# Optimization experiments

Hardware: AMD Instinct MI355X
Metric: run time of the kernel (lower is better)

The kernel has to match this reference:

```python
import jax, jax.numpy as jnp
import numpy as np

D, H, HKV, DH, F, E = 2048, 16, 4, 128, 2048, 8
EPS, THETA = 1e-5, 500000.0
B, S = 1, 512


def _rms(x, w):
    return x * jax.lax.rsqrt(jnp.mean(x * x, -1, keepdims=True) + EPS) * w


def _rope(q, k, pos):
    inv = 1.0 / (THETA ** (jnp.arange(0, DH, 2, dtype=jnp.float32) / DH))
    f = pos.astype(jnp.float32)[..., None] * inv            # (B,S,DH/2)
    cos = jnp.concatenate([jnp.cos(f)] * 2, -1)[:, None]    # (B,1,S,DH)
    sin = jnp.concatenate([jnp.sin(f)] * 2, -1)[:, None]
    def rot(x):
        x1, x2 = jnp.split(x, 2, -1)
        return jnp.concatenate([-x2, x1], -1)
    return q * cos + rot(q) * sin, k * cos + rot(k) * sin


def _forward(hidden_states, attention_mask, position_ids, attn_norm_w, wq, wk, wv, wo,
             ffn_norm_w, router_w, w_gate, w_up, w_down, ws_gate, ws_up, ws_down):
    b, s, _ = hidden_states.shape
    # --- attention block ---
    x = _rms(hidden_states, attn_norm_w)
    q = (x @ wq).reshape(b, s, H, DH).transpose(0, 2, 1, 3)     # (B,H,S,DH)
    k = (x @ wk).reshape(b, s, HKV, DH).transpose(0, 2, 1, 3)   # (B,HKV,S,DH)
    v = (x @ wv).reshape(b, s, HKV, DH).transpose(0, 2, 1, 3)
    q, k = _rope(q, k, position_ids)
    k = jnp.repeat(k, H // HKV, axis=1)
    v = jnp.repeat(v, H // HKV, axis=1)
    scores = jnp.einsum('bhqd,bhkd->bhqk', q, k) / np.float32(np.sqrt(DH))
    causal = jnp.tril(jnp.ones((s, s), bool))
    mask = causal[None, None] & (attention_mask[:, None, None, :] > 0)
    scores = jnp.where(mask, scores, jnp.float32(-1e9))
    p = jax.nn.softmax(scores, axis=-1)
    attn = jnp.einsum('bhqk,bhkd->bhqd', p, v).transpose(0, 2, 1, 3).reshape(b, s, H * DH) @ wo
    h = hidden_states + attn
    # --- MoE block (layer_id even): top-1 sigmoid routing, score scales expert input; shared expert always on ---
    x2 = _rms(h, ffn_norm_w)
    logits = x2 @ router_w                                      # (B,S,E)
    top_idx = jnp.argmax(logits, -1)
    top_score = jax.nn.sigmoid(jnp.max(logits, -1))
    gates = jax.nn.one_hot(top_idx, E, dtype=x2.dtype) * top_score[..., None]  # (B,S,E)
    xin = jnp.einsum('bse,bsd->ebsd', gates, x2)                # scaled dispatch
    g = jax.nn.silu(jnp.einsum('ebsd,edf->ebsf', xin, w_gate))
    u = jnp.einsum('ebsd,edf->ebsf', xin, w_up)
    routed = jnp.einsum('ebsf,efd->bsd', g * u, w_down)
    shared = (jax.nn.silu(x2 @ ws_gate) * (x2 @ ws_up)) @ ws_down
    return h + routed + shared


def setup_inputs() -> dict:
    key = jax.random.key(0)
    ks = jax.random.split(key, 14)
    s = 0.02
    return {
        'hidden_states': jax.random.normal(ks[0], (B, S, D), jnp.float32),
        'attention_mask': jnp.ones((B, S), jnp.int32),
        'position_ids': jnp.broadcast_to(jnp.arange(S, dtype=jnp.int32)[None], (B, S)),
        'attn_norm_w': jnp.ones((D,), jnp.float32),
        'wq': jax.random.normal(ks[1], (D, H * DH), jnp.float32) * s,
        'wk': jax.random.normal(ks[2], (D, HKV * DH), jnp.float32) * s,
        'wv': jax.random.normal(ks[3], (D, HKV * DH), jnp.float32) * s,
        'wo': jax.random.normal(ks[4], (H * DH, D), jnp.float32) * s,
        'ffn_norm_w': jnp.ones((D,), jnp.float32),
        'router_w': jax.random.normal(ks[5], (D, E), jnp.float32) * s,
        'w_gate': jax.random.normal(ks[6], (E, D, F), jnp.float32) * s,
        'w_up': jax.random.normal(ks[7], (E, D, F), jnp.float32) * s,
        'w_down': jax.random.normal(ks[8], (E, F, D), jnp.float32) * s,
        'ws_gate': jax.random.normal(ks[9], (D, F), jnp.float32) * s,
        'ws_up': jax.random.normal(ks[10], (D, F), jnp.float32) * s,
        'ws_down': jax.random.normal(ks[11], (F, D), jnp.float32) * s,
    }


def reference(hidden_states, attention_mask, position_ids, attn_norm_w, wq, wk, wv, wo,
              ffn_norm_w, router_w, w_gate, w_up, w_down, ws_gate, ws_up, ws_down):
    return _forward(hidden_states, attention_mask, position_ids, attn_norm_w, wq, wk, wv, wo,
                    ffn_norm_w, router_w, w_gate, w_up, w_down, ws_gate, ws_up, ws_down)
```

## Files before the change

kernel.cpp:

```cpp
#include <hip/hip_runtime.h>
#include <cstdint>
#include <cstddef>

#define S_LEN 512
#define DMODEL 2048
#define NH 16
#define NKVH 4
#define DHEAD 128
#define FFD 2048
#define NEXP 8

typedef __attribute__((ext_vector_type(8))) short s8v;
typedef __attribute__((ext_vector_type(4))) float f4v;

__device__ __forceinline__ unsigned short f2bf(float f) {
    unsigned int u = __float_as_uint(f);
    unsigned int r = u + 0x7fffu + ((u >> 16) & 1u);
    return (unsigned short)(r >> 16);
}
__device__ __forceinline__ float bf2f(unsigned short h) {
    return __uint_as_float(((unsigned int)h) << 16);
}

__device__ __forceinline__ f4v mfma_bf16(s8v a, s8v b, f4v c) {
    return __builtin_amdgcn_mfma_f32_16x16x32_bf16(a, b, c, 0, 0, 0);
}

__global__ __launch_bounds__(256) void rms_pair_k(const float* __restrict__ x,
                                                  const float* __restrict__ w,
                                                  unsigned short* __restrict__ hi,
                                                  unsigned short* __restrict__ lo) {
    int row = blockIdx.x;
    const float* xr = x + (size_t)row * DMODEL;
    float ss = 0.f;
    for (int i = threadIdx.x; i < DMODEL; i += 256) { float v = xr[i]; ss = fmaf(v, v, ss); }
    for (int off = 32; off > 0; off >>= 1) ss += __shfl_xor(ss, off);
    __shared__ float red[4];
    if ((threadIdx.x & 63) == 0) red[threadIdx.x >> 6] = ss;
    __syncthreads();
    float tot = (red[0] + red[1]) + (red[2] + red[3]);
    float scale = 1.0f / sqrtf(tot * (1.0f / DMODEL) + 1e-5f);
    for (int i = threadIdx.x; i < DMODEL; i += 256) {
        float v = xr[i] * scale * w[i];
        unsigned short hb = f2bf(v);
        hi[(size_t)row * DMODEL + i] = hb;
        lo[(size_t)row * DMODEL + i] = f2bf(v - bf2f(hb));
    }
}

__global__ __launch_bounds__(256) void rms_dual_k(const float* __restrict__ x,
                                                  const float* __restrict__ w,
                                                  float* __restrict__ xf,
                                                  unsigned short* __restrict__ xb) {
    int row = blockIdx.x;
    const float* xr = x + (size_t)row * DMODEL;
    float ss = 0.f;
    for (int i = threadIdx.x; i < DMODEL; i += 256) { float v = xr[i]; ss = fmaf(v, v, ss); }
    for (int off = 32; off > 0; off >>= 1) ss += __shfl_xor(ss, off);
    __shared__ float red[4];
    if ((threadIdx.x & 63) == 0) red[threadIdx.x >> 6] = ss;
    __syncthreads();
    float tot = (red[0] + red[1]) + (red[2] + red[3]);
    float scale = 1.0f / sqrtf(tot * (1.0f / DMODEL) + 1e-5f);
    for (int i = threadIdx.x; i < DMODEL; i += 256) {
        float v = xr[i] * scale * w[i];
        xf[(size_t)row * DMODEL + i] = v;
        xb[(size_t)row * DMODEL + i] = f2bf(v);
    }
}

template <bool SPLIT>
__global__ __launch_bounds__(256) void gemm2_k(const unsigned short* __restrict__ Ahi,
                                               const unsigned short* __restrict__ Alo,
                                               const float* __restrict__ B0,
                                               const float* __restrict__ B1,
                                               float* __restrict__ C0,
                                               float* __restrict__ C1,
                                               int M, int N, int nE, int KS,
                                               const int* __restrict__ lists,
                                               const int* __restrict__ counts,
                                               long long bstride) {
    __shared__ unsigned short Ah[64][40];
    __shared__ unsigned short Al[SPLIT ? 64 : 1][40];
    __shared__ unsigned short Bt[64][40];
    __shared__ unsigned short Bl[SPLIT ? 64 : 1][40];

    int z = blockIdx.z;
    int e = 0;
    if (nE > 1) { e = z % nE; z /= nE; }
    int which = 0;
    if (B1 != nullptr) { which = z & 1; z >>= 1; }
    const int ks = z;

    int myM = M;
    const int* rl = nullptr;
    if (lists) { rl = lists + e * S_LEN; myM = counts[e]; }
    const int m0 = blockIdx.y * 64;
    if (m0 >= myM) return;

    const float* Bp = (which ? B1 : B0) + (long long)e * bstride;
    float* Cp = which ? C1 : C0;
    const int n0 = blockIdx.x * 64;

    const int tid = threadIdx.x;
    const int ar = tid >> 2;
    const int ak = (tid & 3) << 3;
    const int bn = tid & 63;
    const int bk8 = (tid >> 6) << 3;
    const int bc = ((bk8 >> 3) ^ (bn >> 3)) & 3;

    const int arow = m0 + ar;
    const bool avalid = arow < myM;
    const int arow_g = avalid ? (rl ? rl[arow] : arow) : 0;

    const unsigned short* Ahp = Ahi + (size_t)arow_g * DMODEL + ak;
    const unsigned short* Alp = SPLIT ? (Alo + (size_t)arow_g * DMODEL + ak) : nullptr;

    const int lane = tid & 63;
    const int wv = tid >> 6;
    const int wm = wv >> 1;
    const int wn = wv & 1;
    const int lr = lane & 15;
    const int quad = lane >> 4;

    f4v zero = {0.f, 0.f, 0.f, 0.f};
    f4v acc[2][2];
    acc[0][0] = zero; acc[0][1] = zero; acc[1][0] = zero; acc[1][1] = zero;

    const int kslice = DMODEL / KS;
    const int kbeg = ks * kslice;
    const int niter = kslice >> 5;

    for (int it = 0; it < niter; ++it) {
        const int k0 = kbeg + (it << 5);
        uint4 hv = {0, 0, 0, 0};
        uint4 lv = {0, 0, 0, 0};
        if (avalid) {
            hv = *(const uint4*)(Ahp + k0);
            if constexpr (SPLIT) lv = *(const uint4*)(Alp + k0);
        }
        const float* bp = Bp + (size_t)(k0 + bk8) * N + n0 + bn;
        float f[8];
#pragma unroll
        for (int j = 0; j < 8; j++) f[j] = bp[(size_t)j * N];
        unsigned int ph[4], pl[4];
#pragma unroll
        for (int j = 0; j < 4; j++) {
            unsigned short h0 = f2bf(f[2 * j]), h1 = f2bf(f[2 * j + 1]);
            ph[j] = (unsigned int)h0 | ((unsigned int)h1 << 16);
            if constexpr (SPLIT) {
                unsigned short l0 = f2bf(f[2 * j] - bf2f(h0));
                unsigned short l1 = f2bf(f[2 * j + 1] - bf2f(h1));
                pl[j] = (unsigned int)l0 | ((unsigned int)l1 << 16);
            }
        }
        __syncthreads();
        *(uint4*)&Ah[ar][ak] = hv;
        if constexpr (SPLIT) *(uint4*)&Al[ar][ak] = lv;
        *(uint4*)&Bt[bn][bc << 3] = *(uint4*)ph;
        if constexpr (SPLIT) *(uint4*)&Bl[bn][bc << 3] = *(uint4*)pl;
        __syncthreads();
        const int br0 = wn * 32 + lr, br1 = wn * 32 + 16 + lr;
        const int c0 = ((quad ^ (br0 >> 3)) & 3) << 3;
        const int c1 = ((quad ^ (br1 >> 3)) & 3) << 3;
        s8v ah0 = *(const s8v*)&Ah[wm * 32 + lr][quad * 8];
        s8v ah1 = *(const s8v*)&Ah[wm * 32 + 16 + lr][quad * 8];
        s8v bh0 = *(const s8v*)&Bt[br0][c0];
        s8v bh1 = *(const s8v*)&Bt[br1][c1];
        acc[0][0] = mfma_bf16(ah0, bh0, acc[0][0]);
        acc[0][1] = mfma_bf16(ah0, bh1, acc[0][1]);
        acc[1][0] = mfma_bf16(ah1, bh0, acc[1][0]);
        acc[1][1] = mfma_bf16(ah1, bh1, acc[1][1]);
        if constexpr (SPLIT) {
            s8v al0 = *(const s8v*)&Al[wm * 32 + lr][quad * 8];
            s8v al1 = *(const s8v*)&Al[wm * 32 + 16 + lr][quad * 8];
            s8v bl0 = *(const s8v*)&Bl[br0][c0];
            s8v bl1 = *(const s8v*)&Bl[br1][c1];
            acc[0][0] = mfma_bf16(ah0, bl0, acc[0][0]);
            acc[0][0] = mfma_bf16(al0, bh0, acc[0][0]);
            acc[0][1] = mfma_bf16(ah0, bl1, acc[0][1]);
            acc[0][1] = mfma_bf16(al0, bh1, acc[0][1]);
            acc[1][0] = mfma_bf16(ah1, bl0, acc[1][0]);
            acc[1][0] = mfma_bf16(al1, bh0, acc[1][0]);
            acc[1][1] = mfma_bf16(ah1, bl1, acc[1][1]);
            acc[1][1] = mfma_bf16(al1, bh1, acc[1][1]);
        }
    }
#pragma unroll
    for (int t = 0; t < 2; t++) {
#pragma unroll
        for (int u = 0; u < 2; u++) {
#pragma unroll
            for (int r2 = 0; r2 < 4; r2++) {
                int rml = m0 + wm * 32 + t * 16 + quad * 4 + r2;
                if (rml >= myM) continue;
                int rg = rl ? rl[rml] : rml;
                int col = n0 + wn * 32 + u * 16 + lr;
                atomicAdd(&Cp[(size_t)rg * N + col], acc[t][u][r2]);
            }
        }
    }
}

__global__ __launch_bounds__(256) void rope_k(float* __restrict__ qb, float* __restrict__ kb,
                                              const int* __restrict__ pos_ids) {
    int idx = blockIdx.x * 256 + threadIdx.x;
    int i = idx & 63;
    int rest = idx >> 6;
    int head = rest % (NH + NKVH);
    int s = rest / (NH + NKVH);
    if (s >= S_LEN) return;
    float pos = (float)pos_ids[s];
    float inv = (float)exp(-(double)i * (log(500000.0) / 64.0));
    float f = pos * inv;
    float c = cosf(f), sn = sinf(f);
    float* p;
    if (head < NH) p = qb + (size_t)s * (NH * DHEAD) + head * DHEAD;
    else p = kb + (size_t)s * (NKVH * DHEAD) + (head - NH) * DHEAD;
    float x1 = p[i], x2 = p[i + 64];
    p[i] = x1 * c - x2 * sn;
    p[i + 64] = x2 * c + x1 * sn;
}

__global__ __launch_bounds__(256) void attn_k(const float* __restrict__ qb,
                                              const float* __restrict__ kb,
                                              const float* __restrict__ vb,
                                              const int* __restrict__ amask,
                                              unsigned short* __restrict__ ohi,
                                              unsigned short* __restrict__ olo) {
    __shared__ float KV[64][133];
    __shared__ float Qs[16][133];
    __shared__ float Ps[4][4][64];
    const int qt = blockIdx.x;
    const int h = blockIdx.y;
    const int kvh = h >> 2;
    const int tid = threadIdx.x;
    const int w = tid >> 6;
    const int lane = tid & 63;
    const float qsc = 0.08838834764831845f;

    for (int i = tid; i < 16 * 128; i += 256) {
        int r = i >> 7, d = i & 127;
        Qs[r][d] = qb[(size_t)(qt * 16 + r) * (NH * DHEAD) + h * DHEAD + d] * qsc;
    }
    float m_i[4], l_i[4], o0[4], o1[4];
#pragma unroll
    for (int r = 0; r < 4; r++) { m_i[r] = -3.0e38f; l_i[r] = 0.f; o0[r] = 0.f; o1[r] = 0.f; }
    const int ntiles = ((qt * 16 + 15) >> 6) + 1;
    __syncthreads();
    for (int kt = 0; kt < ntiles; kt++) {
        for (int i = tid; i < 64 * 128; i += 256) {
            int r = i >> 7, d = i & 127;
            KV[r][d] = kb[(size_t)(kt * 64 + r) * (NKVH * DHEAD) + kvh * DHEAD + d];
        }
        __syncthreads();
        const int kg = kt * 64 + lane;
        const bool kvalid = (amask[kg] > 0);
        float sc[4] = {0.f, 0.f, 0.f, 0.f};
        for (int d = 0; d < 128; d++) {
            float kval = KV[lane][d];
#pragma unroll
            for (int r = 0; r < 4; r++) sc[r] = fmaf(Qs[w * 4 + r][d], kval, sc[r]);
        }
#pragma unroll
        for (int r = 0; r < 4; r++) {
            const int qg = qt * 16 + w * 4 + r;
            float sr = (kvalid && kg <= qg) ? sc[r] : -1.0e30f;
            float mt = sr;
            for (int off = 32; off > 0; off >>= 1) mt = fmaxf(mt, __shfl_xor(mt, off));
            float mn = fmaxf(m_i[r], mt);
            float p = expf(sr - mn);
            float alpha = expf(m_i[r] - mn);
            float psum = p;
            for (int off = 32; off > 0; off >>= 1) psum += __shfl_xor(psum, off);
            l_i[r] = l_i[r] * alpha + psum;
            m_i[r] = mn;
            o0[r] *= alpha; o1[r] *= alpha;
            Ps[w][r][lane] = p;
        }
        __syncthreads();
        for (int i = tid; i < 64 * 128; i += 256) {
            int r = i >> 7, d = i & 127;
            KV[r][d] = vb[(size_t)(kt * 64 + r) * (NKVH * DHEAD) + kvh * DHEAD + d];
        }
        __syncthreads();
#pragma unroll 4
        for (int j = 0; j < 64; j++) {
            float v0 = KV[j][lane];
            float v1 = KV[j][lane + 64];
#pragma unroll
            for (int r = 0; r < 4; r++) {
                float p = Ps[w][r][j];
                o0[r] = fmaf(p, v0, o0[r]);
                o1[r] = fmaf(p, v1, o1[r]);
            }
        }
        __syncthreads();
    }
#pragma unroll
    for (int r = 0; r < 4; r++) {
        const int qg = qt * 16 + w * 4 + r;
        float linv = 1.0f / l_i[r];
        float a0 = o0[r] * linv, a1 = o1[r] * linv;
        size_t base = (size_t)qg * (NH * DHEAD) + h * DHEAD;
        unsigned short h0 = f2bf(a0), h1 = f2bf(a1);
        ohi[base + lane] = h0;
        ohi[base + lane + 64] = h1;
        olo[base + lane] = f2bf(a0 - bf2f(h0));
        olo[base + lane + 64] = f2bf(a1 - bf2f(h1));
    }
}

__global__ __launch_bounds__(256) void router_k(const float* __restrict__ x2f,
                                                const float* __restrict__ rw,
                                                float* __restrict__ logits) {
    int t = blockIdx.x;
    int e = threadIdx.x >> 5;
    int j = threadIdx.x & 31;
    const float* xr = x2f + (size_t)t * DMODEL;
    float p = 0.f;
    for (int k = j; k < DMODEL; k += 32) p = fmaf(xr[k], rw[(size_t)k * NEXP + e], p);
    for (int off = 16; off > 0; off >>= 1) p += __shfl_xor(p, off);
    if (j == 0) logits[t * NEXP + e] = p;
}

__global__ __launch_bounds__(512) void route_build_k(const float* __restrict__ logits,
                                                     float* __restrict__ tscore,
                                                     int* __restrict__ counts,
                                                     int* __restrict__ lists) {
    int t = threadIdx.x;
    const float* lg = logits + t * NEXP;
    int best = 0;
    float bv = lg[0];
#pragma unroll
    for (int e = 1; e < NEXP; e++) { float v = lg[e]; if (v > bv) { bv = v; best = e; } }
    tscore[t] = 1.0f / (1.0f + expf(-bv));
    int pos = atomicAdd(&counts[best], 1);
    lists[best * S_LEN + pos] = t;
}

__global__ __launch_bounds__(256) void silu_shared_k(const float* __restrict__ G,
                                                     const float* __restrict__ U,
                                                     unsigned short* __restrict__ o) {
    int i = blockIdx.x * 256 + threadIdx.x;
    float g = G[i], u = U[i];
    o[i] = f2bf(g / (1.0f + expf(-g)) * u);
}

__global__ __launch_bounds__(256) void silu_routed_k(const float* __restrict__ G,
                                                     const float* __restrict__ U,
                                                     const float* __restrict__ tscore,
                                                     unsigned short* __restrict__ o) {
    int i = blockIdx.x * 256 + threadIdx.x;
    int t = i >> 11;
    float s = tscore[t];
    float g = s * G[i], u = s * U[i];
    o[i] = f2bf(g / (1.0f + expf(-g)) * u);
}

extern "C" void kernel_launch(void* const* d_in, const int* in_sizes, int n_in,
                              void* d_out, int out_size, void* d_ws, size_t ws_size,
                              hipStream_t stream) {
    const float* hidden = (const float*)d_in[0];
    const int* amask = (const int*)d_in[1];
    const int* posid = (const int*)d_in[2];
    const float* anw = (const float*)d_in[3];
    const float* wq = (const float*)d_in[4];
    const float* wk = (const float*)d_in[5];
    const float* wvv = (const float*)d_in[6];
    const float* wo = (const float*)d_in[7];
    const float* fnw = (const float*)d_in[8];
    const float* rw = (const float*)d_in[9];
    const float* wg = (const float*)d_in[10];
    const float* wu = (const float*)d_in[11];
    const float* wd = (const float*)d_in[12];
    const float* wsg = (const float*)d_in[13];
    const float* wsu = (const float*)d_in[14];
    const float* wsd = (const float*)d_in[15];
    float* out = (float*)d_out;

    char* ws = (char*)d_ws;
    size_t off = 0;
    auto alloc = [&](size_t bytes) -> void* {
        void* p = ws + off;
        off += (bytes + 255) & ~(size_t)255;
        return p;
    };
    unsigned short* x1h = (unsigned short*)alloc((size_t)S_LEN * DMODEL * 2);
    unsigned short* x1l = (unsigned short*)alloc((size_t)S_LEN * DMODEL * 2);
    float* qb = (float*)alloc((size_t)S_LEN * NH * DHEAD * 4);
    float* kb = (float*)alloc((size_t)S_LEN * NKVH * DHEAD * 4);
    float* vb = (float*)alloc((size_t)S_LEN * NKVH * DHEAD * 4);
    unsigned short* ath = (unsigned short*)alloc((size_t)S_LEN * DMODEL * 2);
    unsigned short* atl = (unsigned short*)alloc((size_t)S_LEN * DMODEL * 2);
    float* hbuf = (float*)alloc((size_t)S_LEN * DMODEL * 4);
    float* x2f = (float*)alloc((size_t)S_LEN * DMODEL * 4);
    unsigned short* x2b = (unsigned short*)alloc((size_t)S_LEN * DMODEL * 2);
    float* Gb = (float*)alloc((size_t)S_LEN * FFD * 4);
    float* Ub = (float*)alloc((size_t)S_LEN * FFD * 4);
    float* G2 = (float*)alloc((size_t)S_LEN * FFD * 4);
    float* U2 = (float*)alloc((size_t)S_LEN * FFD * 4);
    unsigned short* smid = (unsigned short*)alloc((size_t)S_LEN * FFD * 2);
    unsigned short* hmid = (unsigned short*)alloc((size_t)S_LEN * FFD * 2);
    float* logits = (float*)alloc((size_t)S_LEN * NEXP * 4);
    float* tscore = (float*)alloc((size_t)S_LEN * 4);
    int* counts = (int*)alloc(NEXP * 4);
    int* lists = (int*)alloc((size_t)NEXP * S_LEN * 4);

    const long long EXP_STRIDE = (long long)DMODEL * FFD;

    hipMemsetAsync(counts, 0, NEXP * 4, stream);
    hipMemsetAsync(qb, 0, (size_t)S_LEN * NH * DHEAD * 4, stream);
    hipMemsetAsync(kb, 0, (size_t)S_LEN * NKVH * DHEAD * 4, stream);
    hipMemsetAsync(vb, 0, (size_t)S_LEN * NKVH * DHEAD * 4, stream);
    hipMemsetAsync(Gb, 0, (size_t)S_LEN * FFD * 4, stream);
    hipMemsetAsync(Ub, 0, (size_t)S_LEN * FFD * 4, stream);
    hipMemsetAsync(G2, 0, (size_t)S_LEN * FFD * 4, stream);
    hipMemsetAsync(U2, 0, (size_t)S_LEN * FFD * 4, stream);
    hipMemcpyAsync(hbuf, hidden, (size_t)S_LEN * DMODEL * 4, hipMemcpyDeviceToDevice, stream);

    rms_pair_k<<<S_LEN, 256, 0, stream>>>(hidden, anw, x1h, x1l);
    gemm2_k<true><<<dim3(32, 8, 4), 256, 0, stream>>>(x1h, x1l, wq, nullptr, qb, nullptr,
                                                      S_LEN, 2048, 1, 4, nullptr, nullptr, 0);
    gemm2_k<true><<<dim3(8, 8, 8), 256, 0, stream>>>(x1h, x1l, wk, wvv, kb, vb,
                                                     S_LEN, 512, 1, 4, nullptr, nullptr, 0);
    rope_k<<<2560, 256, 0, stream>>>(qb, kb, posid);
    attn_k<<<dim3(32, NH), 256, 0, stream>>>(qb, kb, vb, amask, ath, atl);
    gemm2_k<true><<<dim3(32, 8, 4), 256, 0, stream>>>(ath, atl, wo, nullptr, hbuf, nullptr,
                                                      S_LEN, 2048, 1, 4, nullptr, nullptr, 0);

    rms_dual_k<<<S_LEN, 256, 0, stream>>>(hbuf, fnw, x2f, x2b);
    router_k<<<S_LEN, 256, 0, stream>>>(x2f, rw, logits);
    route_build_k<<<1, 512, 0, stream>>>(logits, tscore, counts, lists);

    hipMemcpyAsync(out, hbuf, (size_t)S_LEN * DMODEL * 4, hipMemcpyDeviceToDevice, stream);

    gemm2_k<false><<<dim3(32, 8, 8), 256, 0, stream>>>(x2b, nullptr, wsg, wsu, Gb, Ub,
                                                       S_LEN, FFD, 1, 4, nullptr, nullptr, 0);
    silu_shared_k<<<(S_LEN * FFD) / 256, 256, 0, stream>>>(Gb, Ub, smid);
    gemm2_k<false><<<dim3(32, 8, 4), 256, 0, stream>>>(smid, nullptr, wsd, nullptr, out, nullptr,
                                                       S_LEN, DMODEL, 1, 4, nullptr, nullptr, 0);

    gemm2_k<false><<<dim3(32, 8, 64), 256, 0, stream>>>(x2b, nullptr, wg, wu, G2, U2,
                                                        S_LEN, FFD, NEXP, 4, lists, counts, EXP_STRIDE);
    silu_routed_k<<<(S_LEN * FFD) / 256, 256, 0, stream>>>(G2, U2, tscore, hmid);
    gemm2_k<false><<<dim3(32, 8, 32), 256, 0, stream>>>(hmid, nullptr, wd, nullptr, out, nullptr,
                                                        S_LEN, DMODEL, NEXP, 4, lists, counts, EXP_STRIDE);
}
```

Measured before the change: 819.4 us.

## Replace atomic split-K GEMMs with partial buffers and fuse SwiGLU into gate/up GEMM

The generic split-K GEMM, which accumulated into zeroed buffers, is replaced by specialised kernels. The QKV projection runs as one launch with a 2-way K split into separate partial buffers, which are summed in rope and a v-add kernel. The routed and shared gate/up GEMMs run in a single launch with SiLU and score scaling in the epilogue, which removes the large fp32 G/U intermediates and the separate silu kernels. The down projection writes two partial buffers per path, and a final kernel sums them with the residual. This drops the memsets and memcpys and cuts global traffic, but the gate/up GEMM now loops over the full K with fewer blocks and has more live accumulators.

```diff
diff --git a/kernel.cpp b/kernel.cpp
--- a/kernel.cpp
+++ b/kernel.cpp
@@ -21,7 +21,6 @@
 __device__ __forceinline__ float bf2f(unsigned short h) {
     return __uint_as_float(((unsigned int)h) << 16);
 }
-
 __device__ __forceinline__ f4v mfma_bf16(s8v a, s8v b, f4v c) {
     return __builtin_amdgcn_mfma_f32_16x16x32_bf16(a, b, c, 0, 0, 0);
 }
@@ -48,14 +47,23 @@
     }
 }
 
-__global__ __launch_bounds__(256) void rms_dual_k(const float* __restrict__ x,
-                                                  const float* __restrict__ w,
-                                                  float* __restrict__ xf,
-                                                  unsigned short* __restrict__ xb) {
+__global__ __launch_bounds__(256) void rms_dual2_k(const float* __restrict__ hidden,
+                                                   const float* __restrict__ hs0,
+                                                   const float* __restrict__ hs1,
+                                                   const float* __restrict__ w,
+                                                   float* __restrict__ hbuf,
+                                                   float* __restrict__ xf,
+                                                   unsigned short* __restrict__ xb) {
+    __shared__ float vrow[DMODEL];
     int row = blockIdx.x;
-    const float* xr = x + (size_t)row * DMODEL;
+    size_t base = (size_t)row * DMODEL;
     float ss = 0.f;
-    for (int i = threadIdx.x; i < DMODEL; i += 256) { float v = xr[i]; ss = fmaf(v, v, ss); }
+    for (int i = threadIdx.x; i < DMODEL; i += 256) {
+        float v = hidden[base + i] + hs0[base + i] + hs1[base + i];
+        vrow[i] = v;
+        hbuf[base + i] = v;
+        ss = fmaf(v, v, ss);
+    }
     for (int off = 32; off > 0; off >>= 1) ss += __shfl_xor(ss, off);
     __shared__ float red[4];
     if ((threadIdx.x & 63) == 0) red[threadIdx.x >> 6] = ss;
@@ -63,82 +71,57 @@
     float tot = (red[0] + red[1]) + (red[2] + red[3]);
     float scale = 1.0f / sqrtf(tot * (1.0f / DMODEL) + 1e-5f);
     for (int i = threadIdx.x; i < DMODEL; i += 256) {
-        float v = xr[i] * scale * w[i];
-        xf[(size_t)row * DMODEL + i] = v;
-        xb[(size_t)row * DMODEL + i] = f2bf(v);
-    }
-}
-
-template <bool SPLIT>
-__global__ __launch_bounds__(256) void gemm2_k(const unsigned short* __restrict__ Ahi,
-                                               const unsigned short* __restrict__ Alo,
-                                               const float* __restrict__ B0,
-                                               const float* __restrict__ B1,
-                                               float* __restrict__ C0,
-                                               float* __restrict__ C1,
-                                               int M, int N, int nE, int KS,
-                                               const int* __restrict__ lists,
-                                               const int* __restrict__ counts,
-                                               long long bstride) {
+        float v = vrow[i] * scale * w[i];
+        xf[base + i] = v;
+        xb[base + i] = f2bf(v);
+    }
+}
+
+struct S3Args {
+    const unsigned short* Ahi; const unsigned short* Alo;
+    const float* B0; const float* B1; const float* B2;
+    float* C00; float* C01; float* C10; float* C11; float* C20; float* C21;
+    int N0, N1, N2;
+    int x1, x2;
+};
+
+__global__ __launch_bounds__(256) void gemm_split3_k(S3Args a) {
     __shared__ unsigned short Ah[64][40];
-    __shared__ unsigned short Al[SPLIT ? 64 : 1][40];
+    __shared__ unsigned short Al[64][40];
     __shared__ unsigned short Bt[64][40];
-    __shared__ unsigned short Bl[SPLIT ? 64 : 1][40];
-
-    int z = blockIdx.z;
-    int e = 0;
-    if (nE > 1) { e = z % nE; z /= nE; }
-    int which = 0;
-    if (B1 != nullptr) { which = z & 1; z >>= 1; }
-    const int ks = z;
-
-    int myM = M;
-    const int* rl = nullptr;
-    if (lists) { rl = lists + e * S_LEN; myM = counts[e]; }
+    __shared__ unsigned short Bl[64][40];
+
+    const int x = blockIdx.x;
+    const float* Bp; float* Cp; int N; int n0;
+    if (x < a.x1)      { Bp = a.B0; N = a.N0; n0 = x * 64;
+                         Cp = blockIdx.z ? a.C01 : a.C00; }
+    else if (x < a.x2) { Bp = a.B1; N = a.N1; n0 = (x - a.x1) * 64;
+                         Cp = blockIdx.z ? a.C11 : a.C10; }
+    else               { Bp = a.B2; N = a.N2; n0 = (x - a.x2) * 64;
+                         Cp = blockIdx.z ? a.C21 : a.C20; }
     const int m0 = blockIdx.y * 64;
-    if (m0 >= myM) return;
-
-    const float* Bp = (which ? B1 : B0) + (long long)e * bstride;
-    float* Cp = which ? C1 : C0;
-    const int n0 = blockIdx.x * 64;
+    const int kbeg = blockIdx.z * (DMODEL / 2);
 
     const int tid = threadIdx.x;
-    const int ar = tid >> 2;
-    const int ak = (tid & 3) << 3;
-    const int bn = tid & 63;
-    const int bk8 = (tid >> 6) << 3;
+    const int ar = tid >> 2, ak = (tid & 3) << 3;
+    const int bn = tid & 63, bk8 = (tid >> 6) << 3;
     const int bc = ((bk8 >> 3) ^ (bn >> 3)) & 3;
 
-    const int arow = m0 + ar;
-    const bool avalid = arow < myM;
-    const int arow_g = avalid ? (rl ? rl[arow] : arow) : 0;
-
-    const unsigned short* Ahp = Ahi + (size_t)arow_g * DMODEL + ak;
-    const unsigned short* Alp = SPLIT ? (Alo + (size_t)arow_g * DMODEL + ak) : nullptr;
-
-    const int lane = tid & 63;
-    const int wv = tid >> 6;
-    const int wm = wv >> 1;
-    const int wn = wv & 1;
-    const int lr = lane & 15;
-    const int quad = lane >> 4;
+    const unsigned short* Ahp = a.Ahi + (size_t)(m0 + ar) * DMODEL + ak;
+    const unsigned short* Alp = a.Alo + (size_t)(m0 + ar) * DMODEL + ak;
+
+    const int lane = tid & 63, wv = tid >> 6;
+    const int wm = wv >> 1, wn = wv & 1;
+    const int lr = lane & 15, quad = lane >> 4;
 
     f4v zero = {0.f, 0.f, 0.f, 0.f};
     f4v acc[2][2];
     acc[0][0] = zero; acc[0][1] = zero; acc[1][0] = zero; acc[1][1] = zero;
 
-    const int kslice = DMODEL / KS;
-    const int kbeg = ks * kslice;
-    const int niter = kslice >> 5;
-
-    for (int it = 0; it < niter; ++it) {
+    for (int it = 0; it < 32; ++it) {
         const int k0 = kbeg + (it << 5);
-        uint4 hv = {0, 0, 0, 0};
-        uint4 lv = {0, 0, 0, 0};
-        if (avalid) {
-            hv = *(const uint4*)(Ahp + k0);
-            if constexpr (SPLIT) lv = *(const uint4*)(Alp + k0);
-        }
+        uint4 hv = *(const uint4*)(Ahp + k0);
+        uint4 lv = *(const uint4*)(Alp + k0);
         const float* bp = Bp + (size_t)(k0 + bk8) * N + n0 + bn;
         float f[8];
 #pragma unroll
@@ -148,17 +131,15 @@
         for (int j = 0; j < 4; j++) {
             unsigned short h0 = f2bf(f[2 * j]), h1 = f2bf(f[2 * j + 1]);
             ph[j] = (unsigned int)h0 | ((unsigned int)h1 << 16);
-            if constexpr (SPLIT) {
-                unsigned short l0 = f2bf(f[2 * j] - bf2f(h0));
-                unsigned short l1 = f2bf(f[2 * j + 1] - bf2f(h1));
-                pl[j] = (unsigned int)l0 | ((unsigned int)l1 << 16);
-            }
+            unsigned short l0 = f2bf(f[2 * j] - bf2f(h0));
+            unsigned short l1 = f2bf(f[2 * j + 1] - bf2f(h1));
+            pl[j] = (unsigned int)l0 | ((unsigned int)l1 << 16);
         }
         __syncthreads();
         *(uint4*)&Ah[ar][ak] = hv;
-        if constexpr (SPLIT) *(uint4*)&Al[ar][ak] = lv;
+        *(uint4*)&Al[ar][ak] = lv;
         *(uint4*)&Bt[bn][bc << 3] = *(uint4*)ph;
-        if constexpr (SPLIT) *(uint4*)&Bl[bn][bc << 3] = *(uint4*)pl;
+        *(uint4*)&Bl[bn][bc << 3] = *(uint4*)pl;
         __syncthreads();
         const int br0 = wn * 32 + lr, br1 = wn * 32 + 16 + lr;
         const int c0 = ((quad ^ (br0 >> 3)) & 3) << 3;
@@ -171,39 +152,227 @@
         acc[0][1] = mfma_bf16(ah0, bh1, acc[0][1]);
         acc[1][0] = mfma_bf16(ah1, bh0, acc[1][0]);
         acc[1][1] = mfma_bf16(ah1, bh1, acc[1][1]);
-        if constexpr (SPLIT) {
-            s8v al0 = *(const s8v*)&Al[wm * 32 + lr][quad * 8];
-            s8v al1 = *(const s8v*)&Al[wm * 32 + 16 + lr][quad * 8];
-            s8v bl0 = *(const s8v*)&Bl[br0][c0];
-            s8v bl1 = *(const s8v*)&Bl[br1][c1];
-            acc[0][0] = mfma_bf16(ah0, bl0, acc[0][0]);
-            acc[0][0] = mfma_bf16(al0, bh0, acc[0][0]);
-            acc[0][1] = mfma_bf16(ah0, bl1, acc[0][1]);
-            acc[0][1] = mfma_bf16(al0, bh1, acc[0][1]);
-            acc[1][0] = mfma_bf16(ah1, bl0, acc[1][0]);
-            acc[1][0] = mfma_bf16(al1, bh0, acc[1][0]);
-            acc[1][1] = mfma_bf16(ah1, bl1, acc[1][1]);
-            acc[1][1] = mfma_bf16(al1, bh1, acc[1][1]);
+        s8v al0 = *(const s8v*)&Al[wm * 32 + lr][quad * 8];
+        s8v al1 = *(const s8v*)&Al[wm * 32 + 16 + lr][quad * 8];
+        s8v bl0 = *(const s8v*)&Bl[br0][c0];
+        s8v bl1 = *(const s8v*)&Bl[br1][c1];
+        acc[0][0] = mfma_bf16(ah0, bl0, acc[0][0]);
+        acc[0][0] = mfma_bf16(al0, bh0, acc[0][0]);
+        acc[0][1] = mfma_bf16(ah0, bl1, acc[0][1]);
+        acc[0][1] = mfma_bf16(al0, bh1, acc[0][1]);
+        acc[1][0] = mfma_bf16(ah1, bl0, acc[1][0]);
+        acc[1][0] = mfma_bf16(al1, bh0, acc[1][0]);
+        acc[1][1] = mfma_bf16(ah1, bl1, acc[1][1]);
+        acc[1][1] = mfma_bf16(al1, bh1, acc[1][1]);
+    }
+#pragma unroll
+    for (int t = 0; t < 2; t++)
+#pragma unroll
+        for (int u = 0; u < 2; u++)
+#pragma unroll
+            for (int r2 = 0; r2 < 4; r2++) {
+                int row = m0 + wm * 32 + t * 16 + quad * 4 + r2;
+                int col = n0 + wn * 32 + u * 16 + lr;
+                Cp[(size_t)row * N + col] = acc[t][u][r2];
+            }
+}
+
+__global__ __launch_bounds__(256) void gemm_gu_k(const unsigned short* __restrict__ Ab,
+                                                 const float* __restrict__ wg,
+                                                 const float* __restrict__ wu,
+                                                 const float* __restrict__ wsg,
+                                                 const float* __restrict__ wsu,
+                                                 const float* __restrict__ tscore,
+                                                 const int* __restrict__ lists,
+                                                 const int* __restrict__ counts,
+                                                 unsigned short* __restrict__ hmid,
+                                                 unsigned short* __restrict__ smid) {
+    __shared__ unsigned short Ah[64][40];
+    __shared__ unsigned short Bg[64][40];
+    __shared__ unsigned short Bu[64][40];
+
+    const int e = blockIdx.z;
+    const bool routed = e < NEXP;
+    const int* rl = routed ? lists + e * S_LEN : nullptr;
+    const int myM = routed ? counts[e] : S_LEN;
+    const int m0 = blockIdx.y * 64;
+    if (m0 >= myM) return;
+    const long long ST = (long long)DMODEL * FFD;
+    const float* Bgp = routed ? wg + (long long)e * ST : wsg;
+    const float* Bup = routed ? wu + (long long)e * ST : wsu;
+    unsigned short* outp = routed ? hmid : smid;
+    const int n0 = blockIdx.x * 64;
+
+    const int tid = threadIdx.x;
+    const int ar = tid >> 2, ak = (tid & 3) << 3;
+    const int bn = tid & 63, bk8 = (tid >> 6) << 3;
+    const int bc = ((bk8 >> 3) ^ (bn >> 3)) & 3;
+
+    const int arow = m0 + ar;
+    const bool avalid = arow < myM;
+    const int arow_g = avalid ? (rl ? rl[arow] : arow) : 0;
+    const unsigned short* Ap = Ab + (size_t)arow_g * DMODEL + ak;
+
+    const int lane = tid & 63, wv = tid >> 6;
+    const int wm = wv >> 1, wn = wv & 1;
+    const int lr = lane & 15, quad = lane >> 4;
+
+    f4v zero = {0.f, 0.f, 0.f, 0.f};
+    f4v ag[2][2], au[2][2];
+#pragma unroll
+    for (int t = 0; t < 2; t++)
+#pragma unroll
+        for (int u = 0; u < 2; u++) { ag[t][u] = zero; au[t][u] = zero; }
+
+    for (int it = 0; it < DMODEL / 32; ++it) {
+        const int k0 = it << 5;
+        uint4 hv = {0, 0, 0, 0};
+        if (avalid) hv = *(const uint4*)(Ap + k0);
+        const float* bgp = Bgp + (size_t)(k0 + bk8) * FFD + n0 + bn;
+        const float* bup = Bup + (size_t)(k0 + bk8) * FFD + n0 + bn;
+        float fg[8], fu[8];
+#pragma unroll
+        for (int j = 0; j < 8; j++) fg[j] = bgp[(size_t)j * FFD];
+#pragma unroll
+        for (int j = 0; j < 8; j++) fu[j] = bup[(size_t)j * FFD];
+        unsigned int pg[4], pu[4];
+#pragma unroll
+        for (int j = 0; j < 4; j++) {
+            pg[j] = (unsigned int)f2bf(fg[2 * j]) | ((unsigned int)f2bf(fg[2 * j + 1]) << 16);
+            pu[j] = (unsigned int)f2bf(fu[2 * j]) | ((unsigned int)f2bf(fu[2 * j + 1]) << 16);
         }
-    }
-#pragma unroll
-    for (int t = 0; t < 2; t++) {
-#pragma unroll
-        for (int u = 0; u < 2; u++) {
+        __syncthreads();
+        *(uint4*)&Ah[ar][ak] = hv;
+        *(uint4*)&Bg[bn][bc << 3] = *(uint4*)pg;
+        *(uint4*)&Bu[bn][bc << 3] = *(uint4*)pu;
+        __syncthreads();
+        const int br0 = wn * 32 + lr, br1 = wn * 32 + 16 + lr;
+        const int c0 = ((quad ^ (br0 >> 3)) & 3) << 3;
+        const int c1 = ((quad ^ (br1 >> 3)) & 3) << 3;
+        s8v ah0 = *(const s8v*)&Ah[wm * 32 + lr][quad * 8];
+        s8v ah1 = *(const s8v*)&Ah[wm * 32 + 16 + lr][quad * 8];
+        s8v g0 = *(const s8v*)&Bg[br0][c0];
+        s8v g1 = *(const s8v*)&Bg[br1][c1];
+        s8v u0 = *(const s8v*)&Bu[br0][c0];
+        s8v u1 = *(const s8v*)&Bu[br1][c1];
+        ag[0][0] = mfma_bf16(ah0, g0, ag[0][0]);
+        ag[0][1] = mfma_bf16(ah0, g1, ag[0][1]);
+        ag[1][0] = mfma_bf16(ah1, g0, ag[1][0]);
+        ag[1][1] = mfma_bf16(ah1, g1, ag[1][1]);
+        au[0][0] = mfma_bf16(ah0, u0, au[0][0]);
+        au[0][1] = mfma_bf16(ah0, u1, au[0][1]);
+        au[1][0] = mfma_bf16(ah1, u0, au[1][0]);
+        au[1][1] = mfma_bf16(ah1, u1, au[1][1]);
+    }
+#pragma unroll
+    for (int t = 0; t < 2; t++)
+#pragma unroll
+        for (int u = 0; u < 2; u++)
+#pragma unroll
+            for (int r2 = 0; r2 < 4; r2++) {
+                int rml = m0 + wm * 32 + t * 16 + quad * 4 + r2;
+                if (rml >= myM) continue;
+                int rg = rl ? rl[rml] : rml;
+                float s = routed ? tscore[rg] : 1.0f;
+                float g = s * ag[t][u][r2];
+                float uu = s * au[t][u][r2];
+                float val = g / (1.0f + expf(-g)) * uu;
+                int col = n0 + wn * 32 + u * 16 + lr;
+                outp[(size_t)rg * FFD + col] = f2bf(val);
+            }
+}
+
+__global__ __launch_bounds__(256) void gemm_dn_k(const unsigned short* __restrict__ hmid,
+                                                 const unsigned short* __restrict__ smid,
+                                                 const float* __restrict__ wd,
+                                                 const float* __restrict__ wsd,
+                                                 const int* __restrict__ lists,
+                                                 const int* __restrict__ counts,
+                                                 float* __restrict__ dR0, float* __restrict__ dR1,
+                                                 float* __restrict__ dS0, float* __restrict__ dS1) {
+    __shared__ unsigned short Ah[64][40];
+    __shared__ unsigned short Bt[64][40];
+
+    const int e = blockIdx.z % 9;
+    const int ks = blockIdx.z / 9;
+    const bool routed = e < NEXP;
+    const int* rl = routed ? lists + e * S_LEN : nullptr;
+    const int myM = routed ? counts[e] : S_LEN;
+    const int m0 = blockIdx.y * 64;
+    if (m0 >= myM) return;
+    const long long ST = (long long)FFD * DMODEL;
+    const float* Bp = routed ? wd + (long long)e * ST : wsd;
+    const unsigned short* Ab = routed ? hmid : smid;
+    float* Cp = routed ? (ks ? dR1 : dR0) : (ks ? dS1 : dS0);
+    const int n0 = blockIdx.x * 64;
+    const int kbeg = ks * (FFD / 2);
+
+    const int tid = threadIdx.x;
+    const int ar = tid >> 2, ak = (tid & 3) << 3;
+    const int bn = tid & 63, bk8 = (tid >> 6) << 3;
+    const int bc = ((bk8 >> 3) ^ (bn >> 3)) & 3;
+
+    const int arow = m0 + ar;
+    const bool avalid = arow < myM;
+    const int arow_g = avalid ? (rl ? rl[arow] : arow) : 0;
+    const unsigned short* Ap = Ab + (size_t)arow_g * FFD + ak;
+
+    const int lane = tid & 63, wv = tid >> 6;
+    const int wm = wv >> 1, wn = wv & 1;
+    const int lr = lane & 15, quad = lane >> 4;
+
+    f4v zero = {0.f, 0.f, 0.f, 0.f};
+    f4v acc[2][2];
+    acc[0][0] = zero; acc[0][1] = zero; acc[1][0] = zero; acc[1][1] = zero;
+
+    for (int it = 0; it < 32; ++it) {
+        const int k0 = kbeg + (it << 5);
+        uint4 hv = {0, 0, 0, 0};
+        if (avalid) hv = *(const uint4*)(Ap + k0);
+        const float* bp = Bp + (size_t)(k0 + bk8) * DMODEL + n0 + bn;
+        float f[8];
+#pragma unroll
+        for (int j = 0; j < 8; j++) f[j] = bp[(size_t)j * DMODEL];
+        unsigned int ph[4];
+#pragma unroll
+        for (int j = 0; j < 4; j++)
+            ph[j] = (unsigned int)f2bf(f[2 * j]) | ((unsigned int)f2bf(f[2 * j + 1]) << 16);
+        __syncthreads();
+        *(uint4*)&Ah[ar][ak] = hv;
+        *(uint4*)&Bt[bn][bc << 3] = *(uint4*)ph;
+        __syncthreads();
+        const int br0 = wn * 32 + lr, br1 = wn * 32 + 16 + lr;
+        const int c0 = ((quad ^ (br0 >> 3)) & 3) << 3;
+        const int c1 = ((quad ^ (br1 >> 3)) & 3) << 3;
+        s8v ah0 = *(const s8v*)&Ah[wm * 32 + lr][quad * 8];
+        s8v ah1 = *(const s8v*)&Ah[wm * 32 + 16 + lr][quad * 8];
+        s8v bh0 = *(const s8v*)&Bt[br0][c0];
+        s8v bh1 = *(const s8v*)&Bt[br1][c1];
+        acc[0][0] = mfma_bf16(ah0, bh0, acc[0][0]);
+        acc[0][1] = mfma_bf16(ah0, bh1, acc[0][1]);
+        acc[1][0] = mfma_bf16(ah1, bh0, acc[1][0]);
+        acc[1][1] = mfma_bf16(ah1, bh1, acc[1][1]);
+    }
+#pragma unroll
+    for (int t = 0; t < 2; t++)
+#pragma unroll
+        for (int u = 0; u < 2; u++)
 #pragma unroll
             for (int r2 = 0; r2 < 4; r2++) {
                 int rml = m0 + wm * 32 + t * 16 + quad * 4 + r2;
                 if (rml >= myM) continue;
                 int rg = rl ? rl[rml] : rml;
                 int col = n0 + wn * 32 + u * 16 + lr;
-                atomicAdd(&Cp[(size_t)rg * N + col], acc[t][u][r2]);
+                Cp[(size_t)rg * DMODEL + col] = acc[t][u][r2];
             }
-        }
-    }
-}
-
-__global__ __launch_bounds__(256) void rope_k(float* __restrict__ qb, float* __restrict__ kb,
-                                              const int* __restrict__ pos_ids) {
+}
+
+__global__ __launch_bounds__(256) void rope2_k(const float* __restrict__ qs0,
+                                               const float* __restrict__ qs1,
+                                               const float* __restrict__ ks0,
+                                               const float* __restrict__ ks1,
+                                               float* __restrict__ qb, float* __restrict__ kb,
+                                               const int* __restrict__ pos_ids) {
     int idx = blockIdx.x * 256 + threadIdx.x;
     int i = idx & 63;
     int rest = idx >> 6;
@@ -214,12 +383,48 @@
     float inv = (float)exp(-(double)i * (log(500000.0) / 64.0));
     float f = pos * inv;
     float c = cosf(f), sn = sinf(f);
-    float* p;
-    if (head < NH) p = qb + (size_t)s * (NH * DHEAD) + head * DHEAD;
-    else p = kb + (size_t)s * (NKVH * DHEAD) + (head - NH) * DHEAD;
-    float x1 = p[i], x2 = p[i + 64];
-    p[i] = x1 * c - x2 * sn;
-    p[i + 64] = x2 * c + x1 * sn;
+    size_t o;
+    const float* a; const float* b; float* p;
+    if (head < NH) {
+        o = (size_t)s * (NH * DHEAD) + head * DHEAD;
+        a = qs0; b = qs1; p = qb;
+    } else {
+        o = (size_t)s * (NKVH * DHEAD) + (head - NH) * DHEAD;
+        a = ks0; b = ks1; p = kb;
+    }
+    float x1 = a[o + i] + b[o + i];
+    float x2 = a[o + i + 64] + b[o + i + 64];
+    p[o + i] = x1 * c - x2 * sn;
+    p[o + i + 64] = x2 * c + x1 * sn;
+}
+
+__global__ __launch_bounds__(256) void vadd_k(const float* __restrict__ a,
+                                              const float* __restrict__ b,
+                                              float* __restrict__ o) {
+    int i = blockIdx.x * 256 + threadIdx.x;
+    float4 x = ((const float4*)a)[i];
+    float4 y = ((const float4*)b)[i];
+    float4 r = {x.x + y.x, x.y + y.y, x.z + y.z, x.w + y.w};
+    ((float4*)o)[i] = r;
+}
+
+__global__ __launch_bounds__(256) void final_k(const float* __restrict__ hbuf,
+                                               const float* __restrict__ r0,
+                                               const float* __restrict__ r1,
+                                               const float* __restrict__ s0,
+                                               const float* __restrict__ s1,
+                                               float* __restrict__ out) {
+    int i = blockIdx.x * 256 + threadIdx.x;
+    float4 h = ((const float4*)hbuf)[i];
+    float4 a = ((const float4*)r0)[i];
+    float4 b = ((const float4*)r1)[i];
+    float4 c = ((const float4*)s0)[i];
+    float4 d = ((const float4*)s1)[i];
+    float4 r = {h.x + a.x + b.x + c.x + d.x,
+                h.y + a.y + b.y + c.y + d.y,
+                h.z + a.z + b.z + c.z + d.z,
+                h.w + a.w + b.w + c.w + d.w};
+    ((float4*)out)[i] = r;
 }
 
 __global__ __launch_bounds__(256) void attn_k(const float* __restrict__ qb,
@@ -337,25 +542,6 @@
     tscore[t] = 1.0f / (1.0f + expf(-bv));
     int pos = atomicAdd(&counts[best], 1);
     lists[best * S_LEN + pos] = t;
-}
-
-__global__ __launch_bounds__(256) void silu_shared_k(const float* __restrict__ G,
-                                                     const float* __restrict__ U,
-                                                     unsigned short* __restrict__ o) {
-    int i = blockIdx.x * 256 + threadIdx.x;
-    float g = G[i], u = U[i];
-    o[i] = f2bf(g / (1.0f + expf(-g)) * u);
-}
-
-__global__ __launch_bounds__(256) void silu_routed_k(const float* __restrict__ G,
-                                                     const float* __restrict__ U,
-                                                     const float* __restrict__ tscore,
-                                                     unsigned short* __restrict__ o) {
-    int i = blockIdx.x * 256 + threadIdx.x;
-    int t = i >> 11;
-    float s = tscore[t];
-    float g = s * G[i], u = s * U[i];
-    o[i] = f2bf(g / (1.0f + expf(-g)) * u);
 }
 
 extern "C" void kernel_launch(void* const* d_in, const int* in_sizes, int n_in,
@@ -380,70 +566,67 @@
     float* out = (float*)d_out;
 
     char* ws = (char*)d_ws;
-    size_t off = 0;
-    auto alloc = [&](size_t bytes) -> void* {
-        void* p = ws + off;
-        off += (bytes + 255) & ~(size_t)255;
-        return p;
-    };
-    unsigned short* x1h = (unsigned short*)alloc((size_t)S_LEN * DMODEL * 2);
-    unsigned short* x1l = (unsigned short*)alloc((size_t)S_LEN * DMODEL * 2);
-    float* qb = (float*)alloc((size_t)S_LEN * NH * DHEAD * 4);
-    float* kb = (float*)alloc((size_t)S_LEN * NKVH * DHEAD * 4);
-    float* vb = (float*)alloc((size_t)S_LEN * NKVH * DHEAD * 4);
-    unsigned short* ath = (unsigned short*)alloc((size_t)S_LEN * DMODEL * 2);
-    unsigned short* atl = (unsigned short*)alloc((size_t)S_LEN * DMODEL * 2);
-    float* hbuf = (float*)alloc((size_t)S_LEN * DMODEL * 4);
-    float* x2f = (float*)alloc((size_t)S_LEN * DMODEL * 4);
-    unsigned short* x2b = (unsigned short*)alloc((size_t)S_LEN * DMODEL * 2);
-    float* Gb = (float*)alloc((size_t)S_LEN * FFD * 4);
-    float* Ub = (float*)alloc((size_t)S_LEN * FFD * 4);
-    float* G2 = (float*)alloc((size_t)S_LEN * FFD * 4);
-    float* U2 = (float*)alloc((size_t)S_LEN * FFD * 4);
-    unsigned short* smid = (unsigned short*)alloc((size_t)S_LEN * FFD * 2);
-    unsigned short* hmid = (unsigned short*)alloc((size_t)S_LEN * FFD * 2);
-    float* logits = (float*)alloc((size_t)S_LEN * NEXP * 4);
-    float* tscore = (float*)alloc((size_t)S_LEN * 4);
-    int* counts = (int*)alloc(NEXP * 4);
-    int* lists = (int*)alloc((size_t)NEXP * S_LEN * 4);
-
-    const long long EXP_STRIDE = (long long)DMODEL * FFD;
+    const size_t MB = 1024 * 1024;
+    unsigned short* x1h = (unsigned short*)(ws + 0);
+    unsigned short* x1l = (unsigned short*)(ws + 2 * MB);
+    float* dR0 = (float*)(ws + 0);
+    float* qs0 = (float*)(ws + 4 * MB);
+    float* hs0 = (float*)(ws + 4 * MB);
+    float* dS0 = (float*)(ws + 4 * MB);
+    float* qs1 = (float*)(ws + 8 * MB);
+    float* hs1 = (float*)(ws + 8 * MB);
+    float* dS1 = (float*)(ws + 8 * MB);
+    float* ks0 = (float*)(ws + 12 * MB);
+    float* ks1 = (float*)(ws + 13 * MB);
+    float* vs0 = (float*)(ws + 14 * MB);
+    float* vs1 = (float*)(ws + 15 * MB);
+    float* qb = (float*)(ws + 16 * MB);
+    float* kb = (float*)(ws + 20 * MB);
+    float* vb = (float*)(ws + 21 * MB);
+    unsigned short* ath = (unsigned short*)(ws + 22 * MB);
+    unsigned short* atl = (unsigned short*)(ws + 24 * MB);
+    float* dR1 = (float*)(ws + 22 * MB);
+    float* hbuf = (float*)(ws + 26 * MB);
+    float* x2f = (float*)(ws + 30 * MB);
+    unsigned short* x2b = (unsigned short*)(ws + 34 * MB);
+    unsigned short* hmid = (unsigned short*)(ws + 36 * MB);
+    unsigned short* smid = (unsigned short*)(ws + 38 * MB);
+    float* logits = (float*)(ws + 40 * MB);
+    float* tscore = (float*)(ws + 40 * MB + 16384);
+    int* counts = (int*)(ws + 40 * MB + 20480);
+    int* lists = (int*)(ws + 40 * MB + 24576);
 
     hipMemsetAsync(counts, 0, NEXP * 4, stream);
-    hipMemsetAsync(qb, 0, (size_t)S_LEN * NH * DHEAD * 4, stream);
-    hipMemsetAsync(kb, 0, (size_t)S_LEN * NKVH * DHEAD * 4, stream);
-    hipMemsetAsync(vb, 0, (size_t)S_LEN * NKVH * DHEAD * 4, stream);
-    hipMemsetAsync(Gb, 0, (size_t)S_LEN * FFD * 4, stream);
-    hipMemsetAsync(Ub, 0, (size_t)S_LEN * FFD * 4, stream);
-    hipMemsetAsync(G2, 0, (size_t)S_LEN * FFD * 4, stream);
-    hipMemsetAsync(U2, 0, (size_t)S_LEN * FFD * 4, stream);
-    hipMemcpyAsync(hbuf, hidden, (size_t)S_LEN * DMODEL * 4, hipMemcpyDeviceToDevice, stream);
 
     rms_pair_k<<<S_LEN, 256, 0, stream>>>(hidden, anw, x1h, x1l);
-    gemm2_k<true><<<dim3(32, 8, 4), 256, 0, stream>>>(x1h, x1l, wq, nullptr, qb, nullptr,
-                                                      S_LEN, 2048, 1, 4, nullptr, nullptr, 0);
-    gemm2_k<true><<<dim3(8, 8, 8), 256, 0, stream>>>(x1h, x1l, wk, wvv, kb, vb,
-                                                     S_LEN, 512, 1, 4, nullptr, nullptr, 0);
-    rope_k<<<2560, 256, 0, stream>>>(qb, kb, posid);
+    {
+        S3Args a;
+        a.Ahi = x1h; a.Alo = x1l;
+        a.B0 = wq; a.B1 = wk; a.B2 = wvv;
+        a.C00 = qs0; a.C01 = qs1; a.C10 = ks0; a.C11 = ks1; a.C20 = vs0; a.C21 = vs1;
+        a.N0 = 2048; a.N1 = 512; a.N2 = 512;
+        a.x1 = 32; a.x2 = 40;
+        gemm_split3_k<<<dim3(48, 8, 2), 256, 0, stream>>>(a);
+    }
+    rope2_k<<<2560, 256, 0, stream>>>(qs0, qs1, ks0, ks1, qb, kb, posid);
+    vadd_k<<<(S_LEN * NKVH * DHEAD / 4) / 256, 256, 0, stream>>>(vs0, vs1, vb);
     attn_k<<<dim3(32, NH), 256, 0, stream>>>(qb, kb, vb, amask, ath, atl);
-    gemm2_k<true><<<dim3(32, 8, 4), 256, 0, stream>>>(ath, atl, wo, nullptr, hbuf, nullptr,
-                                                      S_LEN, 2048, 1, 4, nullptr, nullptr, 0);
-
-    rms_dual_k<<<S_LEN, 256, 0, stream>>>(hbuf, fnw, x2f, x2b);
+    {
+        S3Args a;
+        a.Ahi = ath; a.Alo = atl;
+        a.B0 = wo; a.B1 = nullptr; a.B2 = nullptr;
+        a.C00 = hs0; a.C01 = hs1; a.C10 = nullptr; a.C11 = nullptr; a.C20 = nullptr; a.C21 = nullptr;
+        a.N0 = 2048; a.N1 = 0; a.N2 = 0;
+        a.x1 = 32; a.x2 = 40;
+        gemm_split3_k<<<dim3(32, 8, 2), 256, 0, stream>>>(a);
+    }
+    rms_dual2_k<<<S_LEN, 256, 0, stream>>>(hidden, hs0, hs1, fnw, hbuf, x2f, x2b);
+
     router_k<<<S_LEN, 256, 0, stream>>>(x2f, rw, logits);
     route_build_k<<<1, 512, 0, stream>>>(logits, tscore, counts, lists);
-
-    hipMemcpyAsync(out, hbuf, (size_t)S_LEN * DMODEL * 4, hipMemcpyDeviceToDevice, stream);
-
-    gemm2_k<false><<<dim3(32, 8, 8), 256, 0, stream>>>(x2b, nullptr, wsg, wsu, Gb, Ub,
-                                                       S_LEN, FFD, 1, 4, nullptr, nullptr, 0);
-    silu_shared_k<<<(S_LEN * FFD) / 256, 256, 0, stream>>>(Gb, Ub, smid);
-    gemm2_k<false><<<dim3(32, 8, 4), 256, 0, stream>>>(smid, nullptr, wsd, nullptr, out, nullptr,
-                                                       S_LEN, DMODEL, 1, 4, nullptr, nullptr, 0);
-
-    gemm2_k<false><<<dim3(32, 8, 64), 256, 0, stream>>>(x2b, nullptr, wg, wu, G2, U2,
-                                                        S_LEN, FFD, NEXP, 4, lists, counts, EXP_STRIDE);
-    silu_routed_k<<<(S_LEN * FFD) / 256, 256, 0, stream>>>(G2, U2, tscore, hmid);
-    gemm2_k<false><<<dim3(32, 8, 32), 256, 0, stream>>>(hmid, nullptr, wd, nullptr, out, nullptr,
-                                                        S_LEN, DMODEL, NEXP, 4, lists, counts, EXP_STRIDE);
-}
+    gemm_gu_k<<<dim3(32, 8, 9), 256, 0, stream>>>(x2b, wg, wu, wsg, wsu, tscore,
+                                                  lists, counts, hmid, smid);
+    gemm_dn_k<<<dim3(32, 8, 18), 256, 0, stream>>>(hmid, smid, wd, wsd, lists, counts,
+                                                   dR0, dR1, dS0, dS1);
+    final_k<<<(S_LEN * DMODEL / 4) / 256, 256, 0, stream>>>(hbuf, dR0, dR1, dS0, dS1, out);
+}
```

New measurement: 816.0 us. No clear change (-0.4%).
